# Kernel tuning notes

Measured on AMD Instinct MI355X. Metric: run time of the kernel, lower is better.

Reference implementation:

```python
import jax, jax.numpy as jnp
import numpy as np

S, V_SHELL, V_GRID = 4, 90, 642   # shells, dirs/shell, grid vertices
B, F_IN, X, Y, Z = 2, 8, 12, 12, 12


def setup_inputs() -> dict:
    key = jax.random.key(0)
    k1, k2 = jax.random.split(key)
    x = jax.random.normal(k1, (B, F_IN, S * V_SHELL, X, Y, Z), dtype=jnp.float32)
    # per-shell interpolation matrices S2SH @ SH2S[:C], shape [S, V_shell, V_grid]
    W = jax.random.normal(k2, (S, V_SHELL, V_GRID), dtype=jnp.float32) * 0.05
    # shells are concatenated in order -> shell_inverse is sorted with equal counts
    shell_inverse = jnp.repeat(jnp.arange(S, dtype=jnp.int64), V_SHELL)
    return {"x": x, "W": W, "shell_inverse": shell_inverse}


def reference(x, W, shell_inverse):
    # x: [B, F, V', X, Y, Z] with V' = S * V_shell, shell_inverse sorted -> static reshape
    b, f, vp, xx, yy, zz = x.shape
    s, vs, vg = W.shape
    xs = x.reshape(b, f, s, vs, xx, yy, zz)  # per-shell gather (contiguous blocks)
    # einsum 'ijklmn,kp->ijplmn' per shell; output channel block i*F:(i+1)*F -> shell-major
    y = jnp.einsum('bfskxyz,skp->bsfpxyz', xs, W)
    return y.reshape(b, s * f, vg, xx, yy, zz)
```

## Files before the change

kernel.cpp:

```cpp
#include <hip/hip_runtime.h>
#include <cstdint>
#include <cstddef>

#define NB 2
#define NF 8
#define NS 4
#define NK 90
#define NP 642
#define NXYZ 1728
#define MT 64
#define PTILES 11
#define NG 108
#define XT_TASKS (64 * NG * 3)
#define WT_TASKS (NS * PTILES * 4 * 3)
#define GEMM_TASKS (64 * 54 * PTILES)

typedef __attribute__((ext_vector_type(8))) __bf16 bf16x8;
typedef __attribute__((ext_vector_type(4))) float f32x4;
typedef __attribute__((ext_vector_type(4))) uint32_t u32x4;

__device__ __forceinline__ uint32_t pack2bf(float a, float b) {
    uint32_t ua = __builtin_bit_cast(uint32_t, a);
    uint32_t ub = __builtin_bit_cast(uint32_t, b);
    ua += 0x7FFFu + ((ua >> 16) & 1u);
    ub += 0x7FFFu + ((ub >> 16) & 1u);
    return (ua >> 16) | (ub & 0xFFFF0000u);
}

__global__ __launch_bounds__(256) void prep_frag(
    const float* __restrict__ x, const float* __restrict__ Wm,
    uint32_t* __restrict__ ws)
{
    const int tid  = (int)threadIdx.x;
    const int lane = tid & 63;
    const int lr = lane & 15, lg = lane >> 4;
    const int task = (int)blockIdx.x * 4 + (tid >> 6);

    float v[8];
    if (task < XT_TASKS) {
        int t = task;
        const int kk = t % 3;   t /= 3;
        const int g  = t % NG;  t /= NG;
        const int e  = t;
        const int s = e & 3, bf = e >> 2;
        const float* src = x + (size_t)bf * (NS * NK * NXYZ)
                             + (size_t)s * (NK * NXYZ) + g * 16 + lr;
        #pragma unroll
        for (int j = 0; j < 8; ++j) {
            const int k = kk * 32 + lg * 8 + j;
            v[j] = (k < NK) ? src[(size_t)k * NXYZ] : 0.f;
        }
    } else {
        int t = task - XT_TASKS;
        const int kk = t % 3;      t /= 3;
        const int ni = t % 4;      t /= 4;
        const int pt = t % PTILES; t /= PTILES;
        const int s  = t;
        const int p = pt * MT + ni * 16 + lr;
        const float* src = Wm + (size_t)s * (NK * NP) + p;
        #pragma unroll
        for (int j = 0; j < 8; ++j) {
            const int k = kk * 32 + lg * 8 + j;
            v[j] = (k < NK && p < NP) ? src[(size_t)k * NP] : 0.f;
        }
    }
    u32x4 u;
    u.x = pack2bf(v[0], v[1]);
    u.y = pack2bf(v[2], v[3]);
    u.z = pack2bf(v[4], v[5]);
    u.w = pack2bf(v[6], v[7]);
    *(u32x4*)((char*)ws + (size_t)task * 1024 + lane * 16) = u;
}

__global__ __launch_bounds__(256, 4) void gemm_frag(
    const uint32_t* __restrict__ ws, float* __restrict__ y)
{
    const int tid  = (int)threadIdx.x;
    const int lane = tid & 63;
    const int lr = lane & 15, lg = lane >> 4;
    int t = (int)blockIdx.x * 4 + (tid >> 6);
    const int pt  = t % PTILES; t /= PTILES;
    const int n32 = t % 54;     t /= 54;
    const int e   = t;
    const int s = e & 3, bf = e >> 2;

    const char* base  = (const char*)ws + (size_t)lane * 16;
    const char* xbase = base + (size_t)((e * NG + n32 * 2) * 3) * 1024;
    const char* abase = base + (size_t)(XT_TASKS + ((s * PTILES + pt) * 4) * 3) * 1024;

    bf16x8 bfr[2][3], afr[4][3];
    #pragma unroll
    for (int mi = 0; mi < 2; ++mi)
        #pragma unroll
        for (int kk = 0; kk < 3; ++kk)
            bfr[mi][kk] = *(const bf16x8*)(xbase + (mi * 3 + kk) * 1024);
    #pragma unroll
    for (int ni = 0; ni < 4; ++ni)
        #pragma unroll
        for (int kk = 0; kk < 3; ++kk)
            afr[ni][kk] = *(const bf16x8*)(abase + (ni * 3 + kk) * 1024);

    f32x4 acc[2][4];
    #pragma unroll
    for (int mi = 0; mi < 2; ++mi)
        #pragma unroll
        for (int ni = 0; ni < 4; ++ni)
            acc[mi][ni] = (f32x4){0.f, 0.f, 0.f, 0.f};

    #pragma unroll
    for (int kk = 0; kk < 3; ++kk)
        #pragma unroll
        for (int mi = 0; mi < 2; ++mi)
            #pragma unroll
            for (int ni = 0; ni < 4; ++ni)
                acc[mi][ni] = __builtin_amdgcn_mfma_f32_16x16x32_bf16(
                    bfr[mi][kk], afr[ni][kk], acc[mi][ni], 0, 0, 0);

    const int b = bf >> 3, f = bf & 7;
    const size_t chan = (size_t)b * (NS * NF) + (size_t)s * NF + f;
    float* ybase = y + chan * ((size_t)NP * NXYZ) + n32 * 32 + lg * 4;
    #pragma unroll
    for (int ni = 0; ni < 4; ++ni) {
        const int p = pt * MT + ni * 16 + lr;
        if (p < NP) {
            float* dst = ybase + (size_t)p * NXYZ;
            __builtin_nontemporal_store(acc[0][ni], (f32x4*)dst);
            __builtin_nontemporal_store(acc[1][ni], (f32x4*)(dst + 16));
        }
    }
}

#define NT 96
#define NTILES 18
#define KP 96
#define ROWB (KP * 2)

__global__ __launch_bounds__(192, 4) void interp_fallback(
    const float* __restrict__ x, const float* __restrict__ Wm,
    float* __restrict__ y)
{
    __shared__ __align__(16) char As[MT * ROWB];
    __shared__ __align__(16) char Bs[NT * ROWB];

    int blk = (int)blockIdx.x;
    const int nt = blk % NTILES; blk /= NTILES;
    const int f  = blk % NF;     blk /= NF;
    const int s  = blk % NS;     blk /= NS;
    const int b  = blk;
    const int tid = (int)threadIdx.x;
    const int n0 = nt * NT;

    {
        const int c  = tid % NT;
        const int kh = tid / NT;
        const float* xp = x + (((size_t)b * NF + f) * (NS * NK) + (size_t)s * NK) * NXYZ
                            + n0 + c;
        const int cs = (c & 7) << 4;
        #pragma unroll
        for (int kk = 0; kk < 48; kk += 8) {
            const int kb = kh * 48 + kk;
            float v[8];
            #pragma unroll
            for (int j = 0; j < 8; ++j) {
                const int k = kb + j;
                v[j] = (k < NK) ? xp[(size_t)k * NXYZ] : 0.f;
            }
            u32x4 u;
            u.x = pack2bf(v[0], v[1]); u.y = pack2bf(v[2], v[3]);
            u.z = pack2bf(v[4], v[5]); u.w = pack2bf(v[6], v[7]);
            *(u32x4*)(Bs + ((c * ROWB + kb * 2) ^ cs)) = u;
        }
    }

    const int lane = tid & 63;
    const int w  = tid / 64;
    const int lr = lane & 15;
    const int lg = lane >> 4;
    const int ls = (lr & 7) << 4;
    const size_t chan = (size_t)b * (NS * NF) + (size_t)s * NF + f;
    float* ybase = y + chan * ((size_t)NP * NXYZ);
    const int xyzbase = n0 + w * 32 + lg * 4;
    const int ar = tid & 63;
    const int akc = tid >> 6;
    const int ars = (ar & 7) << 4;

    for (int pt = 0; pt < PTILES; ++pt) {
        const int p0 = pt * MT;
        __syncthreads();
        {
            const int p = p0 + ar;
            const bool pv = (p < NP);
            const float* wp = Wm + (size_t)s * NK * NP + p;
            #pragma unroll
            for (int kk = 0; kk < 32; kk += 8) {
                const int kb = akc * 32 + kk;
                float v[8];
                #pragma unroll
                for (int j = 0; j < 8; ++j) {
                    const int k = kb + j;
                    v[j] = (pv && (k < NK)) ? wp[(size_t)k * NP] : 0.f;
                }
                u32x4 u;
                u.x = pack2bf(v[0], v[1]); u.y = pack2bf(v[2], v[3]);
                u.z = pack2bf(v[4], v[5]); u.w = pack2bf(v[6], v[7]);
                *(u32x4*)(As + ((ar * ROWB + kb * 2) ^ ars)) = u;
            }
        }
        __syncthreads();

        f32x4 acc[2][4];
        #pragma unroll
        for (int mi = 0; mi < 2; ++mi)
            #pragma unroll
            for (int ni = 0; ni < 4; ++ni)
                acc[mi][ni] = (f32x4){0.f, 0.f, 0.f, 0.f};

        #pragma unroll
        for (int kk = 0; kk < 3; ++kk) {
            const int kbyte = kk * 64 + lg * 16;
            bf16x8 bxyz[2], ap[4];
            #pragma unroll
            for (int mi = 0; mi < 2; ++mi) {
                const int row = w * 32 + mi * 16 + lr;
                bxyz[mi] = *(const bf16x8*)(Bs + ((row * ROWB + kbyte) ^ ls));
            }
            #pragma unroll
            for (int ni = 0; ni < 4; ++ni) {
                const int row = ni * 16 + lr;
                ap[ni] = *(const bf16x8*)(As + ((row * ROWB + kbyte) ^ ls));
            }
            #pragma unroll
            for (int mi = 0; mi < 2; ++mi)
                #pragma unroll
                for (int ni = 0; ni < 4; ++ni)
                    acc[mi][ni] = __builtin_amdgcn_mfma_f32_16x16x32_bf16(
                        bxyz[mi], ap[ni], acc[mi][ni], 0, 0, 0);
        }

        #pragma unroll
        for (int ni = 0; ni < 4; ++ni) {
            const int p = p0 + ni * 16 + lr;
            if (p < NP) {
                float* dst = ybase + (size_t)p * NXYZ + xyzbase;
                __builtin_nontemporal_store(acc[0][ni], (f32x4*)dst);
                __builtin_nontemporal_store(acc[1][ni], (f32x4*)(dst + 16));
            }
        }
    }
}

extern "C" void kernel_launch(void* const* d_in, const int* in_sizes, int n_in,
                              void* d_out, int out_size, void* d_ws, size_t ws_size,
                              hipStream_t stream) {
    (void)in_sizes; (void)n_in; (void)out_size;
    const float* x  = (const float*)d_in[0];
    const float* Wm = (const float*)d_in[1];
    float* y = (float*)d_out;

    const size_t ws_need = (size_t)(XT_TASKS + WT_TASKS) * 1024;
    if (ws_size >= ws_need) {
        prep_frag<<<(XT_TASKS + WT_TASKS) / 4, 256, 0, stream>>>(x, Wm, (uint32_t*)d_ws);
        gemm_frag<<<GEMM_TASKS / 4, 256, 0, stream>>>((const uint32_t*)d_ws, y);
    } else {
        interp_fallback<<<NB * NS * NF * NTILES, 192, 0, stream>>>(x, Wm, y);
    }
}
```

Measured before the change: 81.27 us.

## Loop over output P-tiles per wave, reusing X fragments with double-buffered W loads

The GEMM kernel now runs one 64-thread wave per (channel, 32-column) pair instead of one wave per (channel, column, p-tile). Each wave keeps its X fragments in registers and loops over all 11 p-tiles, prefetching the next tile's W fragments into a second register buffer while computing the current one. The last partial tile gets a specialised path that only computes and stores the valid rows. This removes the repeated X fragment loads, in exchange for fewer, longer waves and higher register pressure.

```diff
diff --git a/kernel.cpp b/kernel.cpp
--- a/kernel.cpp
+++ b/kernel.cpp
@@ -13,7 +13,6 @@
 #define NG 108
 #define XT_TASKS (64 * NG * 3)
 #define WT_TASKS (NS * PTILES * 4 * 3)
-#define GEMM_TASKS (64 * 54 * PTILES)
 
 typedef __attribute__((ext_vector_type(8))) __bf16 bf16x8;
 typedef __attribute__((ext_vector_type(4))) float f32x4;
@@ -72,60 +71,80 @@
     *(u32x4*)((char*)ws + (size_t)task * 1024 + lane * 16) = u;
 }
 
-__global__ __launch_bounds__(256, 4) void gemm_frag(
+__global__ __launch_bounds__(64, 3) void gemm_loop(
     const uint32_t* __restrict__ ws, float* __restrict__ y)
 {
-    const int tid  = (int)threadIdx.x;
-    const int lane = tid & 63;
+    const int lane = (int)threadIdx.x & 63;
     const int lr = lane & 15, lg = lane >> 4;
-    int t = (int)blockIdx.x * 4 + (tid >> 6);
-    const int pt  = t % PTILES; t /= PTILES;
-    const int n32 = t % 54;     t /= 54;
-    const int e   = t;
-    const int s = e & 3, bf = e >> 2;
-
-    const char* base  = (const char*)ws + (size_t)lane * 16;
-    const char* xbase = base + (size_t)((e * NG + n32 * 2) * 3) * 1024;
-    const char* abase = base + (size_t)(XT_TASKS + ((s * PTILES + pt) * 4) * 3) * 1024;
-
-    bf16x8 bfr[2][3], afr[4][3];
+    int t = (int)blockIdx.x;
+    const int n32 = t % 54;  t /= 54;
+    const int e = t;
+    const int s = e & 3, bfi = e >> 2;
+    const int b = bfi >> 3, f = bfi & 7;
+
+    const char* lbase = (const char*)ws + (size_t)lane * 16;
+    const char* xb = lbase + (size_t)((e * NG + n32 * 2) * 3) * 1024;
+    const char* ab = lbase + (size_t)(XT_TASKS + s * (PTILES * 12)) * 1024;
+
+    bf16x8 B[6];
     #pragma unroll
-    for (int mi = 0; mi < 2; ++mi)
-        #pragma unroll
-        for (int kk = 0; kk < 3; ++kk)
-            bfr[mi][kk] = *(const bf16x8*)(xbase + (mi * 3 + kk) * 1024);
+    for (int i = 0; i < 6; ++i) B[i] = *(const bf16x8*)(xb + i * 1024);
+
+    bf16x8 A0[12], A1[12];
     #pragma unroll
-    for (int ni = 0; ni < 4; ++ni)
-        #pragma unroll
-        for (int kk = 0; kk < 3; ++kk)
-            afr[ni][kk] = *(const bf16x8*)(abase + (ni * 3 + kk) * 1024);
-
-    f32x4 acc[2][4];
+    for (int i = 0; i < 12; ++i) A0[i] = *(const bf16x8*)(ab + i * 1024);
+
+    const size_t chan = (size_t)b * (NS * NF) + (size_t)s * NF + f;
+    float* yrow = y + chan * ((size_t)NP * NXYZ) + (size_t)lr * NXYZ
+                    + n32 * 32 + lg * 4;
+
     #pragma unroll
-    for (int mi = 0; mi < 2; ++mi)
-        #pragma unroll
-        for (int ni = 0; ni < 4; ++ni)
-            acc[mi][ni] = (f32x4){0.f, 0.f, 0.f, 0.f};
-
-    #pragma unroll
-    for (int kk = 0; kk < 3; ++kk)
-        #pragma unroll
-        for (int mi = 0; mi < 2; ++mi)
-            #pragma unroll
-            for (int ni = 0; ni < 4; ++ni)
-                acc[mi][ni] = __builtin_amdgcn_mfma_f32_16x16x32_bf16(
-                    bfr[mi][kk], afr[ni][kk], acc[mi][ni], 0, 0, 0);
-
-    const int b = bf >> 3, f = bf & 7;
-    const size_t chan = (size_t)b * (NS * NF) + (size_t)s * NF + f;
-    float* ybase = y + chan * ((size_t)NP * NXYZ) + n32 * 32 + lg * 4;
-    #pragma unroll
-    for (int ni = 0; ni < 4; ++ni) {
-        const int p = pt * MT + ni * 16 + lr;
-        if (p < NP) {
-            float* dst = ybase + (size_t)p * NXYZ;
-            __builtin_nontemporal_store(acc[0][ni], (f32x4*)dst);
-            __builtin_nontemporal_store(acc[1][ni], (f32x4*)(dst + 16));
+    for (int pt = 0; pt < PTILES; ++pt) {
+        const bf16x8* cur = (pt & 1) ? A1 : A0;
+        bf16x8*       nxt = (pt & 1) ? A0 : A1;
+
+        if (pt < PTILES - 1) {
+            const char* an = ab + (size_t)(pt + 1) * 12 * 1024;
+            const int nload = (pt == PTILES - 2) ? 3 : 12;
+            #pragma unroll
+            for (int i = 0; i < 12; ++i)
+                if (i < nload) nxt[i] = *(const bf16x8*)(an + i * 1024);
+        }
+
+        if (pt < PTILES - 1) {
+            f32x4 acc[2][4];
+            #pragma unroll
+            for (int kk = 0; kk < 3; ++kk)
+                #pragma unroll
+                for (int mi = 0; mi < 2; ++mi)
+                    #pragma unroll
+                    for (int ni = 0; ni < 4; ++ni)
+                        acc[mi][ni] = __builtin_amdgcn_mfma_f32_16x16x32_bf16(
+                            B[mi * 3 + kk], cur[ni * 3 + kk],
+                            kk ? acc[mi][ni] : (f32x4){0.f, 0.f, 0.f, 0.f},
+                            0, 0, 0);
+            float* dbase = yrow + (size_t)(pt * MT) * NXYZ;
+            #pragma unroll
+            for (int ni = 0; ni < 4; ++ni) {
+                float* dst = dbase + (size_t)(ni * 16) * NXYZ;
+                __builtin_nontemporal_store(acc[0][ni], (f32x4*)dst);
+                __builtin_nontemporal_store(acc[1][ni], (f32x4*)(dst + 16));
+            }
+        } else {
+            f32x4 acc0[2];
+            #pragma unroll
+            for (int kk = 0; kk < 3; ++kk)
+                #pragma unroll
+                for (int mi = 0; mi < 2; ++mi)
+                    acc0[mi] = __builtin_amdgcn_mfma_f32_16x16x32_bf16(
+                        B[mi * 3 + kk], cur[kk],
+                        kk ? acc0[mi] : (f32x4){0.f, 0.f, 0.f, 0.f},
+                        0, 0, 0);
+            if (lr < 2) {
+                float* dbase = yrow + (size_t)(pt * MT) * NXYZ;
+                __builtin_nontemporal_store(acc0[0], (f32x4*)dbase);
+                __builtin_nontemporal_store(acc0[1], (f32x4*)(dbase + 16));
+            }
         }
     }
 }
@@ -260,7 +279,7 @@
     const size_t ws_need = (size_t)(XT_TASKS + WT_TASKS) * 1024;
     if (ws_size >= ws_need) {
         prep_frag<<<(XT_TASKS + WT_TASKS) / 4, 256, 0, stream>>>(x, Wm, (uint32_t*)d_ws);
-        gemm_frag<<<GEMM_TASKS / 4, 256, 0, stream>>>((const uint32_t*)d_ws, y);
+        gemm_loop<<<64 * 54, 64, 0, stream>>>((const uint32_t*)d_ws, y);
     } else {
         interp_fallback<<<NB * NS * NF * NTILES, 192, 0, stream>>>(x, Wm, y);
     }
```

After: 111.5 us. 37.2% more time.
